# Performance work log

Hardware: AMD Instinct MI355X
Metric: run time of the kernel (lower is better)

The kernel has to match this reference:

```python
import jax, jax.numpy as jnp
import numpy as np

N = 8000        # nodes
E = 64000       # directed edges (before self-loops)
F_IN = 3201     # node_dim=1 + encoding_dim(128)*25
N_TRAIN = 4000


def setup_inputs() -> dict:
    key = jax.random.key(0)
    k = jax.random.split(key, 4)
    d = {
        'x': jax.random.normal(k[0], (N, F_IN), dtype=jnp.float32),
        'edge_index': jax.random.randint(k[1], (2, E), 0, N),
        'y': jax.random.uniform(k[2], (N,), dtype=jnp.float32),
        'train_idx': jax.random.randint(k[3], (N_TRAIN,), 0, N),
    }
    cnt = [0]
    def w(shape, fan_in):
        cnt[0] += 1
        kk = jax.random.fold_in(jax.random.key(1), cnt[0])
        return (jax.random.normal(kk, shape, dtype=jnp.float32) / np.float32(np.sqrt(fan_in)))
    ones = lambda n: jnp.ones((n,), jnp.float32)
    zeros = lambda n: jnp.zeros((n,), jnp.float32)
    d['bn0_g'] = ones(F_IN); d['bn0_b'] = zeros(F_IN)
    d['W1l'] = w((F_IN, 1024), F_IN); d['W1r'] = w((F_IN, 1024), F_IN)
    d['a1'] = w((2, 512), 512); d['b1'] = zeros(1024)
    d['bn1_g'] = ones(1024); d['bn1_b'] = zeros(1024)
    d['W2l'] = w((1024, 512), 1024); d['W2r'] = w((1024, 512), 1024)
    d['a2'] = w((1, 512), 512); d['b2'] = zeros(512)
    d['bn2_g'] = ones(512); d['bn2_b'] = zeros(512)
    d['W3l'] = w((512, 512), 512); d['W3r'] = w((512, 512), 512)
    d['a3'] = w((1, 512), 512); d['b3'] = zeros(512)
    d['bn3_g'] = ones(512); d['bn3_b'] = zeros(512)
    d['W4l'] = w((512, 512), 512); d['W4r'] = w((512, 512), 512)
    d['a4'] = w((1, 512), 512); d['b4'] = zeros(512)
    d['Wh'] = w((512, 1), 512); d['bh'] = zeros(1)
    return d


def _batchnorm(h, g, b, eps=1e-5):
    # training-mode batch statistics over the node dim
    m = h.mean(axis=0)
    v = h.var(axis=0)
    return (h - m) * jax.lax.rsqrt(v + jnp.float32(eps)) * g + b


def _gatv2(h, src, dst, Wl, Wr, att, bias, n):
    # GATv2Conv with concat heads, softmax over incoming edges, aggr='mean'
    H, C = att.shape
    xl = (h @ Wl).reshape(n, H, C)   # source transform
    xr = (h @ Wr).reshape(n, H, C)   # target transform
    z = jax.nn.leaky_relu(xl[src] + xr[dst], negative_slope=0.2)  # [E,H,C]
    e = jnp.einsum('ehc,hc->eh', z, att)                          # [E,H]
    emax = jax.ops.segment_max(e, dst, num_segments=n)            # segment softmax
    ex = jnp.exp(e - emax[dst])
    denom = jax.ops.segment_sum(ex, dst, num_segments=n)
    alpha = ex / denom[dst]
    agg = jax.ops.segment_sum(alpha[:, :, None] * xl[src], dst, num_segments=n)
    deg = jax.ops.segment_sum(jnp.ones(src.shape[0], h.dtype), dst, num_segments=n)
    return (agg / deg[:, None, None]).reshape(n, H * C) + bias


def reference(x, edge_index, y, train_idx, bn0_g, bn0_b, W1l, W1r, a1, b1,
              bn1_g, bn1_b, W2l, W2r, a2, b2, bn2_g, bn2_b, W3l, W3r, a3, b3,
              bn3_g, bn3_b, W4l, W4r, a4, b4, Wh, bh):
    n = x.shape[0]
    loops = jnp.arange(n, dtype=edge_index.dtype)  # PyG add_self_loops=True
    src = jnp.concatenate([edge_index[0], loops])
    dst = jnp.concatenate([edge_index[1], loops])
    h = _batchnorm(x, bn0_g, bn0_b)
    h = _gatv2(h, src, dst, W1l, W1r, a1, b1, n)          # -> [N,1024]
    h = jax.nn.relu(_batchnorm(h, bn1_g, bn1_b))
    h = _gatv2(h, src, dst, W2l, W2r, a2, b2, n)          # -> [N,512]
    h = jax.nn.relu(_batchnorm(h, bn2_g, bn2_b))
    h = _gatv2(h, src, dst, W3l, W3r, a3, b3, n)
    h = jax.nn.relu(_batchnorm(h, bn3_g, bn3_b))
    h = jax.nn.relu(_gatv2(h, src, dst, W4l, W4r, a4, b4, n))
    pred = jax.nn.sigmoid(h @ Wh + bh)[:, 0]              # [N]
    return pred[train_idx], y[train_idx]
```

## Files before the change

kernel.cpp:

```cpp
#include <hip/hip_runtime.h>
#include <math.h>

typedef __bf16 bf16x8 __attribute__((ext_vector_type(8)));
typedef float f32x16 __attribute__((ext_vector_type(16)));
typedef unsigned short ushort8 __attribute__((ext_vector_type(8)));

__device__ __forceinline__ float bf2f(unsigned short u) {
  union { unsigned int i; float f; } c; c.i = ((unsigned int)u) << 16; return c.f;
}
__device__ __forceinline__ unsigned short f2bf(float f) {
  union { float f; unsigned int i; } c; c.f = f;
  unsigned int r = (c.i + 0x7fffu + ((c.i >> 16) & 1u)) >> 16;
  return (unsigned short)r;
}

__global__ void zero_k(float* __restrict__ statz, int nz, int* __restrict__ deg, int n) {
  int i = blockIdx.x * blockDim.x + threadIdx.x;
  if (i < nz) statz[i] = 0.f;
  if (i < n) deg[i] = 1;
}

__global__ void deg_count_k(const int* __restrict__ dst, int* __restrict__ deg, int e) {
  int i = blockIdx.x * blockDim.x + threadIdx.x;
  if (i < e) atomicAdd(&deg[dst[i]], 1);
}

__global__ void scan_k(const int* __restrict__ deg, int* __restrict__ offsets,
                       int* __restrict__ cursor, int n) {
  __shared__ int sums[1024];
  int tid = threadIdx.x;
  int chunk = (n + 1023) >> 10;
  int base = tid * chunk;
  int s = 0;
  for (int i = 0; i < chunk; ++i) {
    int j = base + i;
    if (j < n) s += deg[j];
  }
  sums[tid] = s;
  __syncthreads();
  for (int off = 1; off < 1024; off <<= 1) {
    int v = (tid >= off) ? sums[tid - off] : 0;
    __syncthreads();
    sums[tid] += v;
    __syncthreads();
  }
  int run = sums[tid] - s;
  for (int i = 0; i < chunk; ++i) {
    int j = base + i;
    if (j < n) {
      offsets[j] = run;
      cursor[j] = run;
      run += deg[j];
    }
  }
  if (tid == 1023) offsets[n] = sums[1023];
}

__global__ void csr_fill_k(const int* __restrict__ src, const int* __restrict__ dst,
                           int* __restrict__ cursor, int* __restrict__ csr_src,
                           int e, int n) {
  int i = blockIdx.x * blockDim.x + threadIdx.x;
  if (i >= e + n) return;
  int s, d;
  if (i < e) { s = src[i]; d = dst[i]; }
  else       { s = i - e;  d = s; }
  int pos = atomicAdd(&cursor[d], 1);
  csr_src[pos] = s;
}

__global__ __launch_bounds__(256)
void stats_convert_k(const float* __restrict__ x, unsigned short* __restrict__ Abf,
                     float* __restrict__ P1, float* __restrict__ P2,
                     int M, int K, int Kp) {
  int c = blockIdx.x * 256 + threadIdx.x;
  if (c >= Kp) return;
  int rows = (M + gridDim.y - 1) / gridDim.y;
  int r0 = blockIdx.y * rows;
  int r1 = min(M, r0 + rows);
  if (c >= K) {
    for (int r = r0; r < r1; ++r) Abf[(size_t)r * Kp + c] = 0;
    return;
  }
  float a = 0.f, b = 0.f;
  int r = r0;
  for (; r + 4 <= r1; r += 4) {
    float v0 = x[(size_t)(r + 0) * K + c];
    float v1 = x[(size_t)(r + 1) * K + c];
    float v2 = x[(size_t)(r + 2) * K + c];
    float v3 = x[(size_t)(r + 3) * K + c];
    a += v0 + v1 + v2 + v3;
    b += v0 * v0 + v1 * v1 + v2 * v2 + v3 * v3;
    Abf[(size_t)(r + 0) * Kp + c] = f2bf(v0);
    Abf[(size_t)(r + 1) * Kp + c] = f2bf(v1);
    Abf[(size_t)(r + 2) * Kp + c] = f2bf(v2);
    Abf[(size_t)(r + 3) * Kp + c] = f2bf(v3);
  }
  for (; r < r1; ++r) {
    float v = x[(size_t)r * K + c];
    a += v; b += v * v;
    Abf[(size_t)r * Kp + c] = f2bf(v);
  }
  P1[(size_t)blockIdx.y * Kp + c] = a;
  P2[(size_t)blockIdx.y * Kp + c] = b;
}

__global__ __launch_bounds__(256)
void col_stats_bf_k(const unsigned short* __restrict__ h, int M, int D,
                    float* __restrict__ P1, float* __restrict__ P2) {
  int c = blockIdx.x * 256 + threadIdx.x;
  if (c >= D) return;
  int rows = (M + gridDim.y - 1) / gridDim.y;
  int r0 = blockIdx.y * rows;
  int r1 = min(M, r0 + rows);
  float a = 0.f, b = 0.f;
  int r = r0;
  for (; r + 4 <= r1; r += 4) {
    float v0 = bf2f(h[(size_t)(r + 0) * D + c]);
    float v1 = bf2f(h[(size_t)(r + 1) * D + c]);
    float v2 = bf2f(h[(size_t)(r + 2) * D + c]);
    float v3 = bf2f(h[(size_t)(r + 3) * D + c]);
    a += v0 + v1 + v2 + v3;
    b += v0 * v0 + v1 * v1 + v2 * v2 + v3 * v3;
  }
  for (; r < r1; ++r) {
    float v = bf2f(h[(size_t)r * D + c]);
    a += v; b += v * v;
  }
  P1[(size_t)blockIdx.y * D + c] = a;
  P2[(size_t)blockIdx.y * D + c] = b;
}

__global__ __launch_bounds__(256)
void coef_k(const float* __restrict__ P1, const float* __restrict__ P2,
            const float* __restrict__ g, const float* __restrict__ b,
            float* __restrict__ outA, float* __restrict__ outC,
            int K, int Kp, int ny, float invM) {
  int cc = threadIdx.x & 63;
  int c = blockIdx.x * 64 + cc;
  int yl = threadIdx.x >> 6;
  __shared__ float red[2][4][64];
  float s1 = 0.f, s2 = 0.f;
  if (c < Kp) {
#pragma unroll 4
    for (int y = yl; y < ny; y += 4) {
      s1 += P1[(size_t)y * Kp + c];
      s2 += P2[(size_t)y * Kp + c];
    }
  }
  red[0][yl][cc] = s1;
  red[1][yl][cc] = s2;
  __syncthreads();
  if (yl == 0 && c < Kp) {
    s1 = red[0][0][cc] + red[0][1][cc] + red[0][2][cc] + red[0][3][cc];
    s2 = red[1][0][cc] + red[1][1][cc] + red[1][2][cc] + red[1][3][cc];
    if (c >= K) { outA[c] = 0.f; outC[c] = 0.f; return; }
    float m = s1 * invM;
    float var = fmaxf(s2 * invM - m * m, 0.f);
    float a = rsqrtf(var + 1e-5f) * g[c];
    outA[c] = a;
    outC[c] = b[c] - m * a;
  }
}

__global__ __launch_bounds__(256)
void bn_apply8_k(const unsigned short* __restrict__ h,
                 const float* __restrict__ aC, const float* __restrict__ cC,
                 unsigned short* __restrict__ outb, size_t total, int D) {
  size_t i = ((size_t)blockIdx.x * 256 + threadIdx.x) * 8;
  if (i >= total) return;
  ushort8 u = *(const ushort8*)(h + i);
  int c = (int)(i % (size_t)D);
  ushort8 o;
#pragma unroll
  for (int j = 0; j < 8; ++j) {
    float v = bf2f(u[j]) * aC[c + j] + cC[c + j];
    o[j] = f2bf(fmaxf(v, 0.f));
  }
  *(ushort8*)(outb + i) = o;
}

__global__ __launch_bounds__(256)
void wconv_pair_k(const float* __restrict__ Wl, const float* __restrict__ Wr,
                  unsigned short* __restrict__ WT, int K, int N, int Kp,
                  const float* __restrict__ coefA) {
  const float* W = blockIdx.z ? Wr : Wl;
  unsigned short* WTo = WT + (size_t)blockIdx.z * N * Kp;
  __shared__ float t[32][33];
  int n0 = blockIdx.x * 32, k0 = blockIdx.y * 32;
  int tx = threadIdx.x & 31, ty = threadIdx.x >> 5;
#pragma unroll
  for (int i = 0; i < 32; i += 8) {
    int k = k0 + ty + i, nn = n0 + tx;
    float v = (k < K && nn < N) ? W[(size_t)k * N + nn] : 0.f;
    t[ty + i][tx] = v;
  }
  float ascale = 1.f;
  if (coefA) {
    int k = k0 + tx;
    ascale = (k < Kp) ? coefA[k] : 0.f;
  }
  __syncthreads();
#pragma unroll
  for (int i = 0; i < 32; i += 8) {
    int nn = n0 + ty + i, k = k0 + tx;
    if (nn < N && k < Kp) {
      WTo[(size_t)nn * Kp + k] = f2bf(t[tx][ty + i] * ascale);
    }
  }
}

__global__ __launch_bounds__(256)
void bias_fold_k(const float* __restrict__ Wl, const float* __restrict__ Wr,
                 const float* __restrict__ coefC, float* __restrict__ bias,
                 int K, int N, int KCH) {
  int col = blockIdx.x * 256 + threadIdx.x;
  if (col >= 2 * N) return;
  const float* W = (col >= N) ? Wr : Wl;
  int nn = (col >= N) ? col - N : col;
  int k0 = blockIdx.y * KCH;
  int k1 = min(K, k0 + KCH);
  float s = 0.f;
  int k = k0;
#pragma unroll 8
  for (; k + 8 <= k1; k += 8) {
    s = fmaf(coefC[k + 0], W[(size_t)(k + 0) * N + nn], s);
    s = fmaf(coefC[k + 1], W[(size_t)(k + 1) * N + nn], s);
    s = fmaf(coefC[k + 2], W[(size_t)(k + 2) * N + nn], s);
    s = fmaf(coefC[k + 3], W[(size_t)(k + 3) * N + nn], s);
    s = fmaf(coefC[k + 4], W[(size_t)(k + 4) * N + nn], s);
    s = fmaf(coefC[k + 5], W[(size_t)(k + 5) * N + nn], s);
    s = fmaf(coefC[k + 6], W[(size_t)(k + 6) * N + nn], s);
    s = fmaf(coefC[k + 7], W[(size_t)(k + 7) * N + nn], s);
  }
  for (; k < k1; ++k) s = fmaf(coefC[k], W[(size_t)k * N + nn], s);
  atomicAdd(&bias[col], s);
}

__global__ __launch_bounds__(256)
void gemm_bf16_k(const unsigned short* __restrict__ A,
                 const unsigned short* __restrict__ Bt,
                 unsigned short* __restrict__ outL, unsigned short* __restrict__ outR,
                 const float* __restrict__ bias, int M, int Nh, int K) {
  __shared__ unsigned short sA[128 * 64];
  __shared__ unsigned short sB[128 * 64];
  const int tid = threadIdx.x;
  const int wave = tid >> 6, lane = tid & 63;
  const int wm = wave >> 1, wn = wave & 1;
  const int l32 = lane & 31, lh = lane >> 5;
  const int row0 = blockIdx.y * 128, col0 = blockIdx.x * 128;

  f32x16 acc[2][2] = {};

  for (int kt = 0; kt < K; kt += 64) {
#pragma unroll
    for (int i = 0; i < 4; ++i) {
      int s = i * 256 + tid;
      int r = s >> 3;
      int g = (s & 7) ^ (r & 7);
      int ra = row0 + r;
      ra = ra < M ? ra : M - 1;
      const unsigned short* ga = A + (size_t)ra * K + (kt + g * 8);
      __builtin_amdgcn_global_load_lds(
          (const __attribute__((address_space(1))) void*)ga,
          (__attribute__((address_space(3))) void*)&sA[s * 8], 16, 0, 0);
      const unsigned short* gb = Bt + (size_t)(col0 + r) * K + (kt + g * 8);
      __builtin_amdgcn_global_load_lds(
          (const __attribute__((address_space(1))) void*)gb,
          (__attribute__((address_space(3))) void*)&sB[s * 8], 16, 0, 0);
    }
    __syncthreads();
#pragma unroll
    for (int s = 0; s < 4; ++s) {
      int g = s * 2 + lh;
      bf16x8 af[2], bfr[2];
#pragma unroll
      for (int t = 0; t < 2; ++t) {
        int r = wm * 64 + t * 32 + l32;
        af[t] = *(const bf16x8*)&sA[(r * 8 + (g ^ (r & 7))) * 8];
        int rb = wn * 64 + t * 32 + l32;
        bfr[t] = *(const bf16x8*)&sB[(rb * 8 + (g ^ (rb & 7))) * 8];
      }
#pragma unroll
      for (int mt = 0; mt < 2; ++mt)
#pragma unroll
        for (int nt = 0; nt < 2; ++nt)
          acc[mt][nt] = __builtin_amdgcn_mfma_f32_32x32x16_bf16(af[mt], bfr[nt], acc[mt][nt], 0, 0, 0);
    }
    __syncthreads();
  }
#pragma unroll
  for (int mt = 0; mt < 2; ++mt) {
#pragma unroll
    for (int nt = 0; nt < 2; ++nt) {
      int col = col0 + wn * 64 + nt * 32 + l32;
      float bv = bias ? bias[col] : 0.f;
      unsigned short* base;
      int cc;
      if (col < Nh) { base = outL; cc = col; }
      else          { base = outR; cc = col - Nh; }
      int rb0 = row0 + wm * 64 + mt * 32 + 4 * lh;
#pragma unroll
      for (int r = 0; r < 16; ++r) {
        int rr = rb0 + (r & 3) + 8 * (r >> 2);
        if (rr < M) base[(size_t)rr * Nh + cc] = f2bf(acc[mt][nt][r] + bv);
      }
    }
  }
}

template <int H>
__global__ __launch_bounds__(256)
void gat_edge_k(const unsigned short* __restrict__ xl, const unsigned short* __restrict__ xr,
                const float* __restrict__ att, const float* __restrict__ bias,
                const int* __restrict__ csr, const int* __restrict__ offsets,
                unsigned short* __restrict__ out, int n, int relu) {
  int gw = (blockIdx.x * 256 + threadIdx.x) >> 6;
  int lane = threadIdx.x & 63;
  if (gw >= n * H) return;
  int node, head;
  if (H == 1) { node = gw; head = 0; }
  else        { node = gw >> 1; head = gw & 1; }
  const int W = H * 512;
  const size_t rowoff = (size_t)node * W + head * 512;
  const size_t choff = (size_t)head * 512 + (size_t)(lane * 8);

  float xrv[8], atv[8];
  {
    ushort8 u = *(const ushort8*)(xr + rowoff + lane * 8);
    const float* ap = att + head * 512 + lane * 8;
#pragma unroll
    for (int j = 0; j < 8; ++j) { xrv[j] = bf2f(u[j]); atv[j] = ap[j]; }
  }
  int p0 = offsets[node], p1 = offsets[node + 1];
  ushort8 u0 = *(const ushort8*)(xl + (size_t)csr[p0] * W + choff);
  ushort8 u1 = u0, u2 = u0;
  if (p0 + 1 < p1) u1 = *(const ushort8*)(xl + (size_t)csr[p0 + 1] * W + choff);
  if (p0 + 2 < p1) u2 = *(const ushort8*)(xl + (size_t)csr[p0 + 2] * W + choff);

  float m = -1e30f, l = 0.f;
  float acc[8];
#pragma unroll
  for (int j = 0; j < 8; ++j) acc[j] = 0.f;
  for (int p = p0; p < p1; ++p) {
    ushort8 u = u0;
    u0 = u1; u1 = u2;
    if (p + 3 < p1) u2 = *(const ushort8*)(xl + (size_t)csr[p + 3] * W + choff);
    float lv[8];
    float e = 0.f;
#pragma unroll
    for (int j = 0; j < 8; ++j) {
      lv[j] = bf2f(u[j]);
      float z = lv[j] + xrv[j];
      z = fmaxf(z, 0.f) + 0.2f * fminf(z, 0.f);
      e = fmaf(z, atv[j], e);
    }
#pragma unroll
    for (int off = 32; off > 0; off >>= 1) e += __shfl_xor(e, off, 64);
    float mn = fmaxf(m, e);
    float corr = __expf(m - mn);
    float w = __expf(e - mn);
    l = l * corr + w;
#pragma unroll
    for (int j = 0; j < 8; ++j) acc[j] = acc[j] * corr + w * lv[j];
    m = mn;
  }
  float inv = 1.f / (l * (float)(p1 - p0));
  const float* bp = bias + head * 512 + lane * 8;
  ushort8 o;
#pragma unroll
  for (int j = 0; j < 8; ++j) {
    float v = acc[j] * inv + bp[j];
    if (relu) v = fmaxf(v, 0.f);
    o[j] = f2bf(v);
  }
  *(ushort8*)(out + rowoff + lane * 8) = o;
}

__global__ void head_gather_k(const unsigned short* __restrict__ h, const float* __restrict__ Wh,
                   const float* __restrict__ bh, const float* __restrict__ y,
                   const int* __restrict__ tidx, float* __restrict__ out, int nt) {
  int gw = (blockIdx.x * 256 + threadIdx.x) >> 6;
  int lane = threadIdx.x & 63;
  if (gw >= nt) return;
  int j = tidx[gw];
  ushort8 u = *(const ushort8*)(h + (size_t)j * 512 + lane * 8);
  const float* wp = Wh + lane * 8;
  float s = 0.f;
#pragma unroll
  for (int q = 0; q < 8; ++q) s = fmaf(bf2f(u[q]), wp[q], s);
#pragma unroll
  for (int off = 32; off > 0; off >>= 1) s += __shfl_xor(s, off, 64);
  if (lane == 0) {
    out[gw] = 1.f / (1.f + __expf(-(s + bh[0])));
    out[nt + gw] = y[j];
  }
}

extern "C" void kernel_launch(void* const* d_in, const int* in_sizes, int n_in,
                              void* d_out, int out_size, void* d_ws, size_t ws_size,
                              hipStream_t stream) {
  const float* x     = (const float*)d_in[0];
  const int*   ei    = (const int*)d_in[1];
  const float* y     = (const float*)d_in[2];
  const int*   tidx  = (const int*)d_in[3];
  const float* bn0_g = (const float*)d_in[4];
  const float* bn0_b = (const float*)d_in[5];
  const float* W1l   = (const float*)d_in[6];
  const float* W1r   = (const float*)d_in[7];
  const float* a1    = (const float*)d_in[8];
  const float* b1    = (const float*)d_in[9];
  const float* bn1_g = (const float*)d_in[10];
  const float* bn1_b = (const float*)d_in[11];
  const float* W2l   = (const float*)d_in[12];
  const float* W2r   = (const float*)d_in[13];
  const float* a2    = (const float*)d_in[14];
  const float* b2    = (const float*)d_in[15];
  const float* bn2_g = (const float*)d_in[16];
  const float* bn2_b = (const float*)d_in[17];
  const float* W3l   = (const float*)d_in[18];
  const float* W3r   = (const float*)d_in[19];
  const float* a3    = (const float*)d_in[20];
  const float* b3    = (const float*)d_in[21];
  const float* bn3_g = (const float*)d_in[22];
  const float* bn3_b = (const float*)d_in[23];
  const float* W4l   = (const float*)d_in[24];
  const float* W4r   = (const float*)d_in[25];
  const float* a4    = (const float*)d_in[26];
  const float* b4    = (const float*)d_in[27];
  const float* Wh    = (const float*)d_in[28];
  const float* bh    = (const float*)d_in[29];
  float* out = (float*)d_out;

  const int n   = in_sizes[2];
  const int E   = in_sizes[1] / 2;
  const int FIN = in_sizes[4];
  const int NT  = in_sizes[3];
  const int ET  = E + n;
  const int KP1 = 3264;
  const int NY0 = 200;
  const int NYS = 160;

  unsigned short* us = (unsigned short*)d_ws;
  const size_t ABF_SZ = (size_t)n * KP1;
  unsigned short* Abf = us;
  unsigned short* hb  = us + ABF_SZ;
  unsigned short* xlb = hb + (size_t)n * 1024;
  unsigned short* xrb = xlb + (size_t)n * 1024;
  float* fp = (float*)(xrb + (size_t)n * 1024);
  float* biasb = fp;           fp += 2048;
  float* coefA = fp;           fp += 3328;
  float* coefC = fp;           fp += 3328;
  float* aC    = fp;           fp += 1024;
  float* cC    = fp;           fp += 1024;
  int* deg     = (int*)fp;
  int* offsets = deg + n;
  int* cursor  = offsets + n + 1;
  int* csr     = cursor + n;
  unsigned short* W1T = hb;
  unsigned short* WT  = Abf + (size_t)n * 1024;
  float* P0a = (float*)hb;
  float* P0b = P0a + (size_t)NY0 * KP1;
  float* Psa = (float*)(Abf + (size_t)n * 1024 + 8ull * 1024 * 1024);
  float* Psb = Psa + (size_t)NYS * 1024;

  const int kZeroCount = 2048;
  int zmax = n > kZeroCount ? n : kZeroCount;
  zero_k<<<(zmax + 255) / 256, 256, 0, stream>>>(biasb, kZeroCount, deg, n);
  deg_count_k<<<(E + 255) / 256, 256, 0, stream>>>(ei + E, deg, E);
  scan_k<<<1, 1024, 0, stream>>>(deg, offsets, cursor, n);
  csr_fill_k<<<(ET + 255) / 256, 256, 0, stream>>>(ei, ei + E, cursor, csr, E, n);

  float invM = 1.f / (float)n;

  {
    dim3 g((KP1 + 255) / 256, NY0);
    stats_convert_k<<<g, 256, 0, stream>>>(x, Abf, P0a, P0b, n, FIN, KP1);
    coef_k<<<(KP1 + 63) / 64, 256, 0, stream>>>(P0a, P0b, bn0_g, bn0_b,
                                                coefA, coefC, FIN, KP1, NY0, invM);
  }

  {
    dim3 gw1(1024 / 32, KP1 / 32, 2);
    wconv_pair_k<<<gw1, 256, 0, stream>>>(W1l, W1r, W1T, FIN, 1024, KP1, coefA);
    dim3 gb(8, (FIN + 127) / 128);
    bias_fold_k<<<gb, 256, 0, stream>>>(W1l, W1r, coefC, biasb, FIN, 1024, 128);
    dim3 g(1024 / 128, (n + 127) / 128);
    gemm_bf16_k<<<g, 256, 0, stream>>>(Abf, W1T, xlb, xlb, biasb, n, 1024, KP1);
    gemm_bf16_k<<<g, 256, 0, stream>>>(Abf, W1T + (size_t)1024 * KP1, xrb, xrb,
                                       biasb + 1024, n, 1024, KP1);
  }
  gat_edge_k<2><<<(n * 2 + 3) / 4, 256, 0, stream>>>(xlb, xrb, a1, b1, csr, offsets, hb, n, 0);
  {
    dim3 g(1024 / 256, NYS);
    col_stats_bf_k<<<g, 256, 0, stream>>>(hb, n, 1024, Psa, Psb);
    coef_k<<<1024 / 64, 256, 0, stream>>>(Psa, Psb, bn1_g, bn1_b, aC, cC, 1024, 1024, NYS, invM);
    bn_apply8_k<<<(int)(((size_t)n * 1024 / 8 + 255) / 256), 256, 0, stream>>>(
        hb, aC, cC, Abf, (size_t)n * 1024, 1024);
  }

  {
    dim3 gw2(512 / 32, 1024 / 32, 2);
    wconv_pair_k<<<gw2, 256, 0, stream>>>(W2l, W2r, WT, 1024, 512, 1024, nullptr);
    dim3 g(1024 / 128, (n + 127) / 128);
    gemm_bf16_k<<<g, 256, 0, stream>>>(Abf, WT, xlb, xrb, nullptr, n, 512, 1024);
  }
  gat_edge_k<1><<<(n + 3) / 4, 256, 0, stream>>>(xlb, xrb, a2, b2, csr, offsets, hb, n, 0);
  {
    dim3 g(512 / 256, NYS);
    col_stats_bf_k<<<g, 256, 0, stream>>>(hb, n, 512, Psa, Psb);
    coef_k<<<512 / 64, 256, 0, stream>>>(Psa, Psb, bn2_g, bn2_b, aC, cC, 512, 512, NYS, invM);
    bn_apply8_k<<<(int)(((size_t)n * 512 / 8 + 255) / 256), 256, 0, stream>>>(
        hb, aC, cC, Abf, (size_t)n * 512, 512);
  }

  {
    dim3 gw3(512 / 32, 512 / 32, 2);
    wconv_pair_k<<<gw3, 256, 0, stream>>>(W3l, W3r, WT, 512, 512, 512, nullptr);
    dim3 g(1024 / 128, (n + 127) / 128);
    gemm_bf16_k<<<g, 256, 0, stream>>>(Abf, WT, xlb, xrb, nullptr, n, 512, 512);
  }
  gat_edge_k<1><<<(n + 3) / 4, 256, 0, stream>>>(xlb, xrb, a3, b3, csr, offsets, hb, n, 0);
  {
    dim3 g(512 / 256, NYS);
    col_stats_bf_k<<<g, 256, 0, stream>>>(hb, n, 512, Psa, Psb);
    coef_k<<<512 / 64, 256, 0, stream>>>(Psa, Psb, bn3_g, bn3_b, aC, cC, 512, 512, NYS, invM);
    bn_apply8_k<<<(int)(((size_t)n * 512 / 8 + 255) / 256), 256, 0, stream>>>(
        hb, aC, cC, Abf, (size_t)n * 512, 512);
  }

  {
    dim3 gw4(512 / 32, 512 / 32, 2);
    wconv_pair_k<<<gw4, 256, 0, stream>>>(W4l, W4r, WT, 512, 512, 512, nullptr);
    dim3 g(1024 / 128, (n + 127) / 128);
    gemm_bf16_k<<<g, 256, 0, stream>>>(Abf, WT, xlb, xrb, nullptr, n, 512, 512);
  }
  gat_edge_k<1><<<(n + 3) / 4, 256, 0, stream>>>(xlb, xrb, a4, b4, csr, offsets, hb, n, 1);

  head_gather_k<<<(NT + 3) / 4, 256, 0, stream>>>(hb, Wh, bh, y, tidx, out, NT);
}
```

Before: 753.3 us.

## Rewrite GEMM with 256-wide tiles, double-buffered LDS and 16x16 MFMA

Replaces the 128x128 single-buffered GEMM with a templated 512-thread kernel using 256-column tiles (256 or 128 rows). It double-buffers LDS so the next k-tile loads while the current one computes, and switches to 16x16x32 MFMA with setprio hints. The first layer's two GEMMs become one launch covering both L and R outputs. This is meant to hide global-load latency and raise data reuse per tile, at the cost of more LDS (up to 128KB per block), higher register pressure and fewer blocks for small-M layers.

```diff
diff --git a/kernel.cpp b/kernel.cpp
--- a/kernel.cpp
+++ b/kernel.cpp
@@ -2,7 +2,7 @@
 #include <math.h>
 
 typedef __bf16 bf16x8 __attribute__((ext_vector_type(8)));
-typedef float f32x16 __attribute__((ext_vector_type(16)));
+typedef float f32x4 __attribute__((ext_vector_type(4)));
 typedef unsigned short ushort8 __attribute__((ext_vector_type(8)));
 
 __device__ __forceinline__ float bf2f(unsigned short u) {
@@ -236,73 +236,111 @@
   atomicAdd(&bias[col], s);
 }
 
-__global__ __launch_bounds__(256)
-void gemm_bf16_k(const unsigned short* __restrict__ A,
-                 const unsigned short* __restrict__ Bt,
-                 unsigned short* __restrict__ outL, unsigned short* __restrict__ outR,
-                 const float* __restrict__ bias, int M, int Nh, int K) {
-  __shared__ unsigned short sA[128 * 64];
-  __shared__ unsigned short sB[128 * 64];
+template <int BMT>
+__global__ __launch_bounds__(512, 2)
+void gemm256_k(const unsigned short* __restrict__ A,
+               const unsigned short* __restrict__ Bt,
+               unsigned short* __restrict__ outL, unsigned short* __restrict__ outR,
+               const float* __restrict__ bias, int M, int Nh, int K) {
+  constexpr int MF = BMT / 32;
+  constexpr int SA = (BMT * 8) / 512;
+  constexpr int SB = 4;
+  __shared__ unsigned short sA[2][BMT * 64];
+  __shared__ unsigned short sB[2][256 * 64];
   const int tid = threadIdx.x;
   const int wave = tid >> 6, lane = tid & 63;
-  const int wm = wave >> 1, wn = wave & 1;
-  const int l32 = lane & 31, lh = lane >> 5;
-  const int row0 = blockIdx.y * 128, col0 = blockIdx.x * 128;
-
-  f32x16 acc[2][2] = {};
-
-  for (int kt = 0; kt < K; kt += 64) {
-#pragma unroll
-    for (int i = 0; i < 4; ++i) {
-      int s = i * 256 + tid;
-      int r = s >> 3;
-      int g = (s & 7) ^ (r & 7);
-      int ra = row0 + r;
-      ra = ra < M ? ra : M - 1;
-      const unsigned short* ga = A + (size_t)ra * K + (kt + g * 8);
+  const int wm = wave >> 2, wn = wave & 3;
+  const int l16 = lane & 15, l4 = lane >> 4;
+  const int row0 = blockIdx.y * BMT, col0 = blockIdx.x * 256;
+  const int NT = K >> 6;
+
+  f32x4 acc[MF][4] = {};
+
+  auto stage = [&](int t, int b) {
+    int kt = t << 6;
+#pragma unroll
+    for (int i = 0; i < SA; ++i) {
+      int slot = i * 512 + tid;
+      int r = slot >> 3;
+      int g = (slot & 7) ^ (r & 7);
+      int ra = row0 + r; ra = ra < M ? ra : M - 1;
+      const unsigned short* ga = A + (size_t)ra * K + kt + g * 8;
       __builtin_amdgcn_global_load_lds(
           (const __attribute__((address_space(1))) void*)ga,
-          (__attribute__((address_space(3))) void*)&sA[s * 8], 16, 0, 0);
-      const unsigned short* gb = Bt + (size_t)(col0 + r) * K + (kt + g * 8);
+          (__attribute__((address_space(3))) void*)&sA[b][slot * 8], 16, 0, 0);
+    }
+#pragma unroll
+    for (int i = 0; i < SB; ++i) {
+      int slot = i * 512 + tid;
+      int r = slot >> 3;
+      int g = (slot & 7) ^ (r & 7);
+      const unsigned short* gb = Bt + (size_t)(col0 + r) * K + kt + g * 8;
       __builtin_amdgcn_global_load_lds(
           (const __attribute__((address_space(1))) void*)gb,
-          (__attribute__((address_space(3))) void*)&sB[s * 8], 16, 0, 0);
-    }
-    __syncthreads();
-#pragma unroll
-    for (int s = 0; s < 4; ++s) {
-      int g = s * 2 + lh;
-      bf16x8 af[2], bfr[2];
-#pragma unroll
-      for (int t = 0; t < 2; ++t) {
-        int r = wm * 64 + t * 32 + l32;
-        af[t] = *(const bf16x8*)&sA[(r * 8 + (g ^ (r & 7))) * 8];
-        int rb = wn * 64 + t * 32 + l32;
-        bfr[t] = *(const bf16x8*)&sB[(rb * 8 + (g ^ (rb & 7))) * 8];
+          (__attribute__((address_space(3))) void*)&sB[b][slot * 8], 16, 0, 0);
+    }
+  };
+
+  stage(0, 0);
+  if (NT > 1) stage(1, 1);
+  if constexpr (BMT == 256) asm volatile("s_waitcnt vmcnt(8)" ::: "memory");
+  else                      asm volatile("s_waitcnt vmcnt(6)" ::: "memory");
+  __builtin_amdgcn_sched_barrier(0);
+  __builtin_amdgcn_s_barrier();
+
+  int cur = 0;
+  for (int t = 0; t < NT; ++t) {
+#pragma unroll
+    for (int s = 0; s < 2; ++s) {
+      bf16x8 afr[MF], bfr[4];
+#pragma unroll
+      for (int i = 0; i < MF; ++i) {
+        int rl = wm * (BMT / 2) + i * 16 + l16;
+        int g = s * 4 + l4;
+        afr[i] = *(const bf16x8*)&sA[cur][rl * 64 + ((g ^ (rl & 7)) << 3)];
       }
 #pragma unroll
-      for (int mt = 0; mt < 2; ++mt)
-#pragma unroll
-        for (int nt = 0; nt < 2; ++nt)
-          acc[mt][nt] = __builtin_amdgcn_mfma_f32_32x32x16_bf16(af[mt], bfr[nt], acc[mt][nt], 0, 0, 0);
-    }
-    __syncthreads();
-  }
-#pragma unroll
-  for (int mt = 0; mt < 2; ++mt) {
-#pragma unroll
-    for (int nt = 0; nt < 2; ++nt) {
-      int col = col0 + wn * 64 + nt * 32 + l32;
+      for (int j = 0; j < 4; ++j) {
+        int rl = wn * 64 + j * 16 + l16;
+        int g = s * 4 + l4;
+        bfr[j] = *(const bf16x8*)&sB[cur][rl * 64 + ((g ^ (rl & 7)) << 3)];
+      }
+      __builtin_amdgcn_s_setprio(1);
+#pragma unroll
+      for (int i = 0; i < MF; ++i)
+#pragma unroll
+        for (int j = 0; j < 4; ++j)
+          acc[i][j] = __builtin_amdgcn_mfma_f32_16x16x32_bf16(afr[i], bfr[j], acc[i][j], 0, 0, 0);
+      __builtin_amdgcn_s_setprio(0);
+    }
+    if (t + 1 == NT) break;
+    __builtin_amdgcn_s_barrier();
+    if (t + 2 < NT) {
+      stage(t + 2, cur);
+      if constexpr (BMT == 256) asm volatile("s_waitcnt vmcnt(8)" ::: "memory");
+      else                      asm volatile("s_waitcnt vmcnt(6)" ::: "memory");
+    } else {
+      asm volatile("s_waitcnt vmcnt(0)" ::: "memory");
+    }
+    __builtin_amdgcn_sched_barrier(0);
+    __builtin_amdgcn_s_barrier();
+    cur ^= 1;
+  }
+
+#pragma unroll
+  for (int i = 0; i < MF; ++i) {
+#pragma unroll
+    for (int j = 0; j < 4; ++j) {
+      int col = col0 + wn * 64 + j * 16 + l16;
       float bv = bias ? bias[col] : 0.f;
-      unsigned short* base;
-      int cc;
+      unsigned short* base; int cc;
       if (col < Nh) { base = outL; cc = col; }
       else          { base = outR; cc = col - Nh; }
-      int rb0 = row0 + wm * 64 + mt * 32 + 4 * lh;
-#pragma unroll
-      for (int r = 0; r < 16; ++r) {
-        int rr = rb0 + (r & 3) + 8 * (r >> 2);
-        if (rr < M) base[(size_t)rr * Nh + cc] = f2bf(acc[mt][nt][r] + bv);
+      int rb = row0 + wm * (BMT / 2) + i * 16 + l4 * 4;
+#pragma unroll
+      for (int r = 0; r < 4; ++r) {
+        int rr = rb + r;
+        if (rr < M) base[(size_t)rr * Nh + cc] = f2bf(acc[i][j][r] + bv);
       }
     }
   }
@@ -484,10 +522,8 @@
     wconv_pair_k<<<gw1, 256, 0, stream>>>(W1l, W1r, W1T, FIN, 1024, KP1, coefA);
     dim3 gb(8, (FIN + 127) / 128);
     bias_fold_k<<<gb, 256, 0, stream>>>(W1l, W1r, coefC, biasb, FIN, 1024, 128);
-    dim3 g(1024 / 128, (n + 127) / 128);
-    gemm_bf16_k<<<g, 256, 0, stream>>>(Abf, W1T, xlb, xlb, biasb, n, 1024, KP1);
-    gemm_bf16_k<<<g, 256, 0, stream>>>(Abf, W1T + (size_t)1024 * KP1, xrb, xrb,
-                                       biasb + 1024, n, 1024, KP1);
+    dim3 g(2048 / 256, (n + 255) / 256);
+    gemm256_k<256><<<g, 512, 0, stream>>>(Abf, W1T, xlb, xrb, biasb, n, 1024, KP1);
   }
   gat_edge_k<2><<<(n * 2 + 3) / 4, 256, 0, stream>>>(xlb, xrb, a1, b1, csr, offsets, hb, n, 0);
   {
@@ -501,8 +537,8 @@
   {
     dim3 gw2(512 / 32, 1024 / 32, 2);
     wconv_pair_k<<<gw2, 256, 0, stream>>>(W2l, W2r, WT, 1024, 512, 1024, nullptr);
-    dim3 g(1024 / 128, (n + 127) / 128);
-    gemm_bf16_k<<<g, 256, 0, stream>>>(Abf, WT, xlb, xrb, nullptr, n, 512, 1024);
+    dim3 g(1024 / 256, (n + 127) / 128);
+    gemm256_k<128><<<g, 512, 0, stream>>>(Abf, WT, xlb, xrb, nullptr, n, 512, 1024);
   }
   gat_edge_k<1><<<(n + 3) / 4, 256, 0, stream>>>(xlb, xrb, a2, b2, csr, offsets, hb, n, 0);
   {
@@ -516,8 +552,8 @@
   {
     dim3 gw3(512 / 32, 512 / 32, 2);
     wconv_pair_k<<<gw3, 256, 0, stream>>>(W3l, W3r, WT, 512, 512, 512, nullptr);
-    dim3 g(1024 / 128, (n + 127) / 128);
-    gemm_bf16_k<<<g, 256, 0, stream>>>(Abf, WT, xlb, xrb, nullptr, n, 512, 512);
+    dim3 g(1024 / 256, (n + 127) / 128);
+    gemm256_k<128><<<g, 512, 0, stream>>>(Abf, WT, xlb, xrb, nullptr, n, 512, 512);
   }
   gat_edge_k<1><<<(n + 3) / 4, 256, 0, stream>>>(xlb, xrb, a3, b3, csr, offsets, hb, n, 0);
   {
@@ -531,8 +567,8 @@
   {
     dim3 gw4(512 / 32, 512 / 32, 2);
     wconv_pair_k<<<gw4, 256, 0, stream>>>(W4l, W4r, WT, 512, 512, 512, nullptr);
-    dim3 g(1024 / 128, (n + 127) / 128);
-    gemm_bf16_k<<<g, 256, 0, stream>>>(Abf, WT, xlb, xrb, nullptr, n, 512, 512);
+    dim3 g(1024 / 256, (n + 127) / 128);
+    gemm256_k<128><<<g, 512, 0, stream>>>(Abf, WT, xlb, xrb, nullptr, n, 512, 512);
   }
   gat_edge_k<1><<<(n + 3) / 4, 256, 0, stream>>>(xlb, xrb, a4, b4, csr, offsets, hb, n, 1);
 
```

Result: faster. 726.9 us (-3.5%).
